# Kernel tuning notes

Hardware: AMD Instinct MI355X
Metric: run time of the kernel (lower is better)

Reference implementation:

```python
import jax, jax.numpy as jnp
import numpy as np

R, B, S, H, E, P = 8, 16, 512, 1024, 32, 4  # roles, batch, seq(=max_seq_len=char_len), hidden, entities, spans/entity


def setup_inputs() -> dict:
    key = jax.random.key(0)
    ks = jax.random.split(key, 12)
    w = 0.02
    return {
        "role_labels": jax.random.randint(ks[0], (R, B), 0, S),
        "summar_role_embedding": jax.random.normal(ks[1], (R, B, S, H), jnp.float32),
        "token_embedding": jax.random.normal(ks[2], (B, S, H), jnp.float32),
        "entities_embedding": jax.random.normal(ks[3], (B, S, H), jnp.float32),
        "token_mask": jnp.ones((B, S), jnp.float32),
        "entity_mask": jnp.ones((B, S), jnp.float32),
        # padded ragged spans: sort (start,end) so start<=end; empty spans write nothing
        "entity_spans": jnp.sort(jax.random.randint(ks[4], (B, E, P, 2), 0, S), axis=-1),
        # -1 encodes Python None entries in the original ragged maps
        "char2token": jax.random.randint(ks[5], (B, S), -1, S),
        "entity2token": jax.random.randint(ks[6], (B, S), -1, E),
        "single_w": jax.random.normal(ks[7], (3 * H, 1), jnp.float32) * w,
        "single_b": jnp.zeros((1,), jnp.float32),
        "multi_w": jax.random.normal(ks[8], (3 * H, 1), jnp.float32) * w,
        "multi_b": jnp.zeros((1,), jnp.float32),
        "answer_w": jax.random.normal(ks[9], (2 * H, H), jnp.float32) * w,
        "answer_b": jnp.zeros((H,), jnp.float32),
    }


def reference(role_labels, summar_role_embedding, token_embedding, entities_embedding,
              token_mask, entity_mask, entity_spans, char2token, entity2token,
              single_w, single_b, multi_w, multi_b, answer_w, answer_b):
    Bd, Sd, Hd = token_embedding.shape
    Ed = entity_spans.shape[1]
    brow = jnp.arange(Bd)[:, None]
    cvalid = char2token >= 0
    cidx = jnp.where(cvalid, char2token, 0)
    evalid = entity2token >= 0
    eidx = jnp.where(evalid, entity2token, 0)
    pos = jnp.arange(Sd)[None, None, None, :]  # [1,1,1,S]
    # span coverage mask [B,E,P,S]; assumes non-overlapping gold spans (matches sequential writes)
    cover = ((pos >= entity_spans[..., 0:1]) & (pos < entity_spans[..., 1:2])).astype(token_embedding.dtype)
    mask_sum = token_mask.sum()

    def step(pre_answer, xs):
        sr_emb, labels = xs
        s_logit = jnp.concatenate([sr_emb, token_embedding, pre_answer], -1) @ single_w + single_b  # [B,S,1]
        m_logit = jnp.concatenate([sr_emb, entities_embedding, pre_answer], -1) @ multi_w + multi_b
        # nn.Softmax() with no dim on a 3D tensor uses legacy dim=0 (batch axis)
        s_pred = jax.nn.softmax(s_logit, axis=0)[..., 0]  # [B,S]
        m_pred = jax.nn.softmax(m_logit, axis=0)[..., 0]
        # scatter-add char scores onto token positions / entity ids
        pred_token_ids = jnp.zeros((Bd, Sd), s_pred.dtype).at[brow, cidx].add(jnp.where(cvalid, s_pred, 0.0))
        entity_scores = jnp.zeros((Bd, Ed), m_pred.dtype).at[brow, eidx].add(jnp.where(evalid, m_pred, 0.0))
        # broadcast entity score over its spans
        pred_entity_ids = jnp.einsum('beps,be->bs', cover, entity_scores)
        merged = jnp.maximum(pred_token_ids, pred_entity_ids)  # max-merge [B,S]
        # gather merged scores back to char positions
        arg_emb = jnp.where(cvalid, jnp.take_along_axis(merged, cidx, axis=1), 0.0)[..., None]  # [B,S,1]
        curr = token_embedding * arg_emb
        new_pre = jnp.concatenate([curr, pre_answer], -1) @ answer_w + answer_b
        # CrossEntropyLoss(merged [B,C=S], labels [B]) -> scalar mean, then * token_mask.sum()
        nll = -jnp.take_along_axis(jax.nn.log_softmax(merged, -1), labels[:, None], axis=1).mean()
        return new_pre, (merged, nll * mask_sum)

    pre0 = jnp.zeros_like(token_embedding)
    _, (pred_arg_ids, losses) = jax.lax.scan(step, pre0, (summar_role_embedding, role_labels))
    return losses.sum(), pred_arg_ids
```

## Files before the change

### kernel.cpp

```cpp
#include <hip/hip_runtime.h>
#include <stdint.h>

#define R_ 8
#define B_ 16
#define S_ 512
#define H_ 1024
#define E_ 32
#define P_ 4
#define M_ (B_*S_)
#define SRB2_ 1024
#define TOKB_ 512
#define ENTB_ 512

__device__ __forceinline__ float dot4(float4 a, float4 b){
  return a.x*b.x + a.y*b.y + a.z*b.z + a.w*b.w;
}

__device__ __forceinline__ void group_barrier(int* cnt, int nblk){
  __syncthreads();
  if (threadIdx.x == 0){
    __threadfence();
    __hip_atomic_fetch_add(cnt, 1, __ATOMIC_RELEASE, __HIP_MEMORY_SCOPE_AGENT);
    while (__hip_atomic_load(cnt, __ATOMIC_ACQUIRE, __HIP_MEMORY_SCOPE_AGENT) < nblk)
      __builtin_amdgcn_s_sleep(8);
    __threadfence();
  }
  __syncthreads();
}

__global__ __launch_bounds__(256) void vec_chain_kernel(
    int k, const float* __restrict__ aw, const float* __restrict__ ab,
    const float* __restrict__ sw, const float* __restrict__ mw,
    float* __restrict__ a_s, float* __restrict__ a_m,
    float* __restrict__ V, float* __restrict__ betas)
{
  int w = (int)((blockIdx.x * blockDim.x + threadIdx.x) >> 6);
  int lane = threadIdx.x & 63;
  const float* as_k = (k == 0) ? (sw + 2*H_) : (a_s + (size_t)k*H_);
  const float* am_k = (k == 0) ? (mw + 2*H_) : (a_m + (size_t)k*H_);
  if (w < H_){
    const float* w1 = aw + (size_t)w * H_;
    const float* w2 = aw + (size_t)(H_ + w) * H_;
    float vs = 0.f, vm = 0.f, ns = 0.f, nm = 0.f;
    #pragma unroll
    for (int i = 0; i < 4; i++){
      int c = i*256 + lane*4;
      float4 r1 = *(const float4*)(w1 + c);
      float4 r2 = *(const float4*)(w2 + c);
      float4 xs = *(const float4*)(as_k + c);
      float4 xm = *(const float4*)(am_k + c);
      vs += dot4(r1, xs); vm += dot4(r1, xm);
      ns += dot4(r2, xs); nm += dot4(r2, xm);
    }
    #pragma unroll
    for (int m = 32; m >= 1; m >>= 1){
      vs += __shfl_xor(vs, m, 64); vm += __shfl_xor(vm, m, 64);
      ns += __shfl_xor(ns, m, 64); nm += __shfl_xor(nm, m, 64);
    }
    if (lane == 0){
      V[(size_t)k*H_ + w]       = vs;
      V[(size_t)(7 + k)*H_ + w] = vm;
      a_s[(size_t)(k+1)*H_ + w] = ns;
      a_m[(size_t)(k+1)*H_ + w] = nm;
    }
  } else if (w == H_ || w == H_ + 1){
    const float* av = (w == H_) ? as_k : am_k;
    float d = 0.f;
    #pragma unroll
    for (int i = 0; i < 4; i++){
      int c = i*256 + lane*4;
      d += dot4(*(const float4*)(ab + c), *(const float4*)(av + c));
    }
    #pragma unroll
    for (int m = 32; m >= 1; m >>= 1) d += __shfl_xor(d, m, 64);
    if (lane == 0) betas[(w == H_ ? 0 : 8) + k] = d;
  }
}

__global__ __launch_bounds__(256) void dots_staged_kernel(
    const float* __restrict__ sr, const float* __restrict__ tok,
    const float* __restrict__ ent, const float* __restrict__ sw,
    const float* __restrict__ mw, const float* __restrict__ V,
    const float* __restrict__ tmask,
    float* __restrict__ sr_s, float* __restrict__ sr_m,
    float* __restrict__ tok_s, float* __restrict__ ent_m,
    float* __restrict__ G, float* __restrict__ PS,
    float* __restrict__ msum, float* __restrict__ out)
{
  __shared__ float lds[8*1024];
  const int blk  = blockIdx.x;
  const int lane = threadIdx.x & 63;
  const int lw   = threadIdx.x >> 6;
  const int co   = lane * 4;

  if (blk < SRB2_){
    float4 ws4[4], wm4[4];
    #pragma unroll
    for (int i = 0; i < 4; i++){
      ws4[i] = *(const float4*)(sw + i*256 + co);
      wm4[i] = *(const float4*)(mw + i*256 + co);
    }
    auto STAGE = [&](int bufI, int h){
      int row = (blk + (h >> 1)*SRB2_)*8 + (h & 1)*4 + lw;
      const float* gb = sr + (size_t)row * H_;
      float* lb = lds + bufI*4096 + lw*1024;
      #pragma unroll
      for (int p = 0; p < 4; ++p){
        __builtin_amdgcn_global_load_lds(
            (const __attribute__((address_space(1))) unsigned int*)(gb + p*256 + lane*4),
            (__attribute__((address_space(3))) unsigned int*)(lb + p*256), 16, 0, 0);
      }
    };
    STAGE(0, 0);
    for (int h = 0; h < 16; ++h){
      if (h < 15){
        STAGE((h + 1) & 1, h + 1);
        asm volatile("s_waitcnt vmcnt(4)" ::: "memory");
      } else {
        asm volatile("s_waitcnt vmcnt(0)" ::: "memory");
      }
      const float* lrow = lds + (h & 1)*4096 + lw*1024;
      float a0 = 0.f, a1 = 0.f;
      #pragma unroll
      for (int i = 0; i < 4; i++){
        float4 v = *(const float4*)(lrow + i*256 + co);
        a0 += dot4(v, ws4[i]);
        a1 += dot4(v, wm4[i]);
      }
      #pragma unroll
      for (int m = 32; m >= 1; m >>= 1){
        a0 += __shfl_xor(a0,m,64); a1 += __shfl_xor(a1,m,64);
      }
      int row = (blk + (h >> 1)*SRB2_)*8 + (h & 1)*4 + lw;
      if (lane == 0){ sr_s[row] = a0; sr_m[row] = a1; }
    }
  } else if (blk < SRB2_ + TOKB_){
    const int gw = (blk - SRB2_)*4 + lw;
    const int h  = gw & 1;
    const int r0 = gw >> 1;
    if (h == 0){
      for (int it = 0; it < 8; ++it){
        int rr = r0 + it*1024;
        const float* rp = tok + (size_t)rr * H_;
        float acc[8];
        #pragma unroll
        for (int q = 0; q < 8; q++) acc[q] = 0.f;
        #pragma unroll
        for (int i = 0; i < 4; i++){
          int c = i*256 + co;
          float4 v = *(const float4*)(rp + c);
          acc[0] += dot4(v, *(const float4*)(sw + H_ + c));
          #pragma unroll
          for (int q = 0; q < 7; q++)
            acc[q+1] += dot4(v, *(const float4*)(V + (size_t)q*H_ + c));
        }
        #pragma unroll
        for (int m = 32; m >= 1; m >>= 1)
          #pragma unroll
          for (int q = 0; q < 8; q++) acc[q] += __shfl_xor(acc[q],m,64);
        if (lane == 0){
          tok_s[rr] = acc[0];
          #pragma unroll
          for (int q = 0; q < 7; q++) G[(size_t)q*M_ + rr] = acc[q+1];
        }
      }
    } else {
      for (int it = 0; it < 8; ++it){
        int rr = r0 + it*1024;
        const float* rp = tok + (size_t)rr * H_;
        float acc[7];
        #pragma unroll
        for (int q = 0; q < 7; q++) acc[q] = 0.f;
        #pragma unroll
        for (int i = 0; i < 4; i++){
          int c = i*256 + co;
          float4 v = *(const float4*)(rp + c);
          #pragma unroll
          for (int q = 0; q < 7; q++)
            acc[q] += dot4(v, *(const float4*)(V + (size_t)(7+q)*H_ + c));
        }
        #pragma unroll
        for (int m = 32; m >= 1; m >>= 1)
          #pragma unroll
          for (int q = 0; q < 7; q++) acc[q] += __shfl_xor(acc[q],m,64);
        if (lane == 0){
          #pragma unroll
          for (int q = 0; q < 7; q++) G[(size_t)(7+q)*M_ + rr] = acc[q];
        }
      }
    }
  } else {
    const int eb = blk - SRB2_ - TOKB_;
    const int gt = eb*256 + threadIdx.x;
    if (gt < 32768) ((float4*)PS)[gt] = make_float4(0.f,0.f,0.f,0.f);
    if (eb == 0 && lw == 0){
      float s = 0.f;
      #pragma unroll
      for (int i = 0; i < 32; i++){
        float4 v = ((const float4*)tmask)[i*64 + lane];
        s += v.x + v.y + v.z + v.w;
      }
      #pragma unroll
      for (int m = 32; m >= 1; m >>= 1) s += __shfl_xor(s, m, 64);
      if (lane == 0){ msum[0] = s; out[0] = 0.f; }
    }
    const int ew = eb*4 + lw;
    float4 wmh[4];
    #pragma unroll
    for (int i = 0; i < 4; i++) wmh[i] = *(const float4*)(mw + H_ + i*256 + co);
    #pragma unroll
    for (int it = 0; it < 4; ++it){
      int rr = ew + it*2048;
      const float* rp = ent + (size_t)rr * H_;
      float a0 = 0.f;
      #pragma unroll
      for (int i = 0; i < 4; i++)
        a0 += dot4(*(const float4*)(rp + i*256 + co), wmh[i]);
      #pragma unroll
      for (int m = 32; m >= 1; m >>= 1) a0 += __shfl_xor(a0,m,64);
      if (lane == 0) ent_m[rr] = a0;
    }
  }
}

__global__ __launch_bounds__(512) void roles_kernel(
    const float* __restrict__ sr_s, const float* __restrict__ sr_m,
    const float* __restrict__ tok_s, const float* __restrict__ ent_m,
    const float* __restrict__ G, const float* __restrict__ betas,
    const float* __restrict__ sb, const float* __restrict__ mb,
    const int* __restrict__ c2t, const int* __restrict__ e2t,
    const int* __restrict__ spans, const int* __restrict__ labels,
    const float* __restrict__ msum, float* __restrict__ out,
    float* __restrict__ xlog, float* __restrict__ PS, int* bar)
{
  __shared__ float pta[S_];
  __shared__ float merged[S_];
  __shared__ float es[E_];
  __shared__ float red[8];
  __shared__ int   spn[E_*P_*2];
  const int b = blockIdx.x;
  const int t = threadIdx.x;
  const int bs = b*S_ + t;
  const int wid = t >> 6, lane = t & 63;

  if (t < E_*P_*2) spn[t] = spans[b*(E_*P_*2) + t];
  const int c_own = c2t[bs];
  const int e_own = e2t[bs];
  const float sb0 = sb[0], mb0 = mb[0];
  const float msumv = msum[0];
  const float tok_sv = tok_s[bs], ent_mv = ent_m[bs];
  float bsum_s = 0.f, bsum_m = 0.f;

  for (int r = 0; r < R_; ++r){
    pta[t] = 0.f;
    if (t < E_) es[t] = 0.f;

    float sl[B_], ml[B_];
    if (r == 0){
      #pragma unroll
      for (int bb = 0; bb < B_; bb++){
        int q = bb*S_ + t;
        sl[bb] = sr_s[q] + tok_s[q] + sb0;
        ml[bb] = sr_m[q] + ent_m[q] + mb0;
      }
    } else {
      const float* xc = xlog + (size_t)(r & 1) * (2*M_);
      #pragma unroll
      for (int bb = 0; bb < B_; bb++){
        sl[bb] = xc[bb*S_ + t];
        ml[bb] = xc[M_ + bb*S_ + t];
      }
    }
    float smax = -1e30f, mmax = -1e30f;
    #pragma unroll
    for (int bb = 0; bb < B_; bb++){ smax = fmaxf(smax, sl[bb]); mmax = fmaxf(mmax, ml[bb]); }
    float ssum = 0.f, msv = 0.f;
    #pragma unroll
    for (int bb = 0; bb < B_; bb++){ ssum += __expf(sl[bb]-smax); msv += __expf(ml[bb]-mmax); }
    float spv = __expf(sl[b]-smax) / ssum;
    float mpv = __expf(ml[b]-mmax) / msv;

    __syncthreads();
    if (c_own >= 0) atomicAdd(&pta[c_own], spv);
    if (e_own >= 0) atomicAdd(&es[e_own], mpv);
    __syncthreads();

    float pei = 0.f;
    #pragma unroll
    for (int e = 0; e < E_; e++){
      float sc = es[e];
      #pragma unroll
      for (int p = 0; p < P_; p++){
        int st = spn[e*8 + p*2], en = spn[e*8 + p*2 + 1];
        if (t >= st && t < en) pei += sc;
      }
    }
    float mg = fmaxf(pta[t], pei);
    merged[t] = mg;
    out[1 + (size_t)r*M_ + bs] = mg;
    __syncthreads();

    float ah_r = (c_own >= 0) ? merged[c_own] : 0.f;

    float mx = mg;
    #pragma unroll
    for (int k = 32; k >= 1; k >>= 1) mx = fmaxf(mx, __shfl_xor(mx, k, 64));
    if (lane == 0) red[wid] = mx;
    __syncthreads();
    float gmx = red[0];
    #pragma unroll
    for (int i = 1; i < 8; i++) gmx = fmaxf(gmx, red[i]);
    float se = __expf(mg - gmx);
    #pragma unroll
    for (int k = 32; k >= 1; k >>= 1) se += __shfl_xor(se, k, 64);
    __syncthreads();
    if (lane == 0) red[wid] = se;
    __syncthreads();
    if (t == 0){
      float tot = 0.f;
      #pragma unroll
      for (int i = 0; i < 8; i++) tot += red[i];
      float lse = gmx + __logf(tot);
      int lbl = labels[r*B_ + b];
      float nll = lse - merged[lbl];
      atomicAdd(out, nll * msumv * (1.0f/16.0f));
    }

    if (r < 7){
      bsum_s += betas[r]; bsum_m += betas[8 + r];
      float ps_next = 0.f, pm_next = 0.f;
      for (int q = r + 1; q <= 7; q++){
        float gs = G[(size_t)(q-1-r)*M_ + bs];
        float gm = G[(size_t)(7 + q-1-r)*M_ + bs];
        float ns = PS[((size_t)q*2 + 0)*M_ + bs] + ah_r * gs;
        float nm = PS[((size_t)q*2 + 1)*M_ + bs] + ah_r * gm;
        PS[((size_t)q*2 + 0)*M_ + bs] = ns;
        PS[((size_t)q*2 + 1)*M_ + bs] = nm;
        if (q == r + 1){ ps_next = ns; pm_next = nm; }
      }
      float xn = sr_s[(size_t)((r+1)*B_ + b)*S_ + t] + tok_sv + ps_next + sb0 + bsum_s;
      float yn = sr_m[(size_t)((r+1)*B_ + b)*S_ + t] + ent_mv + pm_next + mb0 + bsum_m;
      float* xn_buf = xlog + (size_t)((r+1) & 1) * (2*M_);
      xn_buf[bs] = xn;
      xn_buf[M_ + bs] = yn;
      group_barrier(&bar[r], 16);
    }
  }
}

extern "C" void kernel_launch(void* const* d_in, const int* in_sizes, int n_in,
                              void* d_out, int out_size, void* d_ws, size_t ws_size,
                              hipStream_t stream){
  (void)in_sizes; (void)n_in; (void)out_size; (void)ws_size;
  const int*   labels = (const int*)  d_in[0];
  const float* sr     = (const float*)d_in[1];
  const float* tok    = (const float*)d_in[2];
  const float* ent    = (const float*)d_in[3];
  const float* tmask  = (const float*)d_in[4];
  const int*   spans  = (const int*)  d_in[6];
  const int*   c2t    = (const int*)  d_in[7];
  const int*   e2t    = (const int*)  d_in[8];
  const float* sw     = (const float*)d_in[9];
  const float* sb     = (const float*)d_in[10];
  const float* mw     = (const float*)d_in[11];
  const float* mb     = (const float*)d_in[12];
  const float* aw     = (const float*)d_in[13];
  const float* ab     = (const float*)d_in[14];
  float* out = (float*)d_out;
  char*  ws  = (char*)d_ws;

  size_t o = 0;
  auto take = [&](size_t bytes){ size_t c = o; o += (bytes + 255) & ~(size_t)255; return c; };
  float* sr_s  = (float*)(ws + take((size_t)R_*B_*S_*4));
  float* sr_m  = (float*)(ws + take((size_t)R_*B_*S_*4));
  float* tok_s = (float*)(ws + take((size_t)B_*S_*4));
  float* ent_m = (float*)(ws + take((size_t)B_*S_*4));
  float* a_s   = (float*)(ws + take((size_t)8*H_*4));
  float* a_m   = (float*)(ws + take((size_t)8*H_*4));
  float* V     = (float*)(ws + take((size_t)14*H_*4));
  float* betas = (float*)(ws + take(64));
  float* G     = (float*)(ws + take((size_t)14*M_*4));
  float* PS    = (float*)(ws + take((size_t)8*2*M_*4));
  float* xlog  = (float*)(ws + take((size_t)2*2*M_*4));
  float* msum  = (float*)(ws + take(256));
  int*   bar   = (int*)  (ws + take(64));

  hipMemsetAsync(bar, 0, 64, stream);
  for (int k = 0; k < 7; k++)
    vec_chain_kernel<<<257, 256, 0, stream>>>(k, aw, ab, sw, mw, a_s, a_m, V, betas);
  dots_staged_kernel<<<2048, 256, 0, stream>>>(sr, tok, ent, sw, mw, V, tmask,
                                               sr_s, sr_m, tok_s, ent_m, G, PS, msum, out);
  roles_kernel<<<16, 512, 0, stream>>>(sr_s, sr_m, tok_s, ent_m, G, betas,
                                       sb, mb, c2t, e2t, spans, labels, msum, out,
                                       xlog, PS, bar);
}
```

Measured before the change: 170.5 us.

## Spread summary-role dot products across the serial vector-chain launches

```diff
diff --git a/kernel.cpp b/kernel.cpp
--- a/kernel.cpp
+++ b/kernel.cpp
@@ -11,6 +11,8 @@
 #define SRB2_ 1024
 #define TOKB_ 512
 #define ENTB_ 512
+#define CHB_  257
+#define SLICE_ 8192
 
 __device__ __forceinline__ float dot4(float4 a, float4 b){
   return a.x*b.x + a.y*b.y + a.z*b.z + a.w*b.w;
@@ -28,52 +30,115 @@
   __syncthreads();
 }
 
-__global__ __launch_bounds__(256) void vec_chain_kernel(
-    int k, const float* __restrict__ aw, const float* __restrict__ ab,
-    const float* __restrict__ sw, const float* __restrict__ mw,
+__global__ __launch_bounds__(256) void hybrid_kernel(
+    int k,
+    const float* __restrict__ sr, const float* __restrict__ aw,
+    const float* __restrict__ ab, const float* __restrict__ sw,
+    const float* __restrict__ mw,
     float* __restrict__ a_s, float* __restrict__ a_m,
-    float* __restrict__ V, float* __restrict__ betas)
+    float* __restrict__ V, float* __restrict__ betas,
+    float* __restrict__ sr_s, float* __restrict__ sr_m)
 {
-  int w = (int)((blockIdx.x * blockDim.x + threadIdx.x) >> 6);
-  int lane = threadIdx.x & 63;
-  const float* as_k = (k == 0) ? (sw + 2*H_) : (a_s + (size_t)k*H_);
-  const float* am_k = (k == 0) ? (mw + 2*H_) : (a_m + (size_t)k*H_);
-  if (w < H_){
-    const float* w1 = aw + (size_t)w * H_;
-    const float* w2 = aw + (size_t)(H_ + w) * H_;
-    float vs = 0.f, vm = 0.f, ns = 0.f, nm = 0.f;
+  __shared__ float lds[8*1024];
+  const int blk  = blockIdx.x;
+  const int lane = threadIdx.x & 63;
+  const int lw   = threadIdx.x >> 6;
+  const int co   = lane * 4;
+
+  if (blk < CHB_){
+    int w = blk*4 + lw;
+    const float* as_k = (k == 0) ? (sw + 2*H_) : (a_s + (size_t)k*H_);
+    const float* am_k = (k == 0) ? (mw + 2*H_) : (a_m + (size_t)k*H_);
+    if (w < H_){
+      const float* w1 = aw + (size_t)w * H_;
+      const float* w2 = aw + (size_t)(H_ + w) * H_;
+      float vs = 0.f, vm = 0.f, ns = 0.f, nm = 0.f;
+      #pragma unroll
+      for (int i = 0; i < 4; i++){
+        int c = i*256 + co;
+        float4 r1 = *(const float4*)(w1 + c);
+        float4 r2 = *(const float4*)(w2 + c);
+        float4 xs = *(const float4*)(as_k + c);
+        float4 xm = *(const float4*)(am_k + c);
+        vs += dot4(r1, xs); vm += dot4(r1, xm);
+        ns += dot4(r2, xs); nm += dot4(r2, xm);
+      }
+      #pragma unroll
+      for (int m = 32; m >= 1; m >>= 1){
+        vs += __shfl_xor(vs, m, 64); vm += __shfl_xor(vm, m, 64);
+        ns += __shfl_xor(ns, m, 64); nm += __shfl_xor(nm, m, 64);
+      }
+      if (lane == 0){
+        V[(size_t)k*H_ + w]       = vs;
+        V[(size_t)(7 + k)*H_ + w] = vm;
+        a_s[(size_t)(k+1)*H_ + w] = ns;
+        a_m[(size_t)(k+1)*H_ + w] = nm;
+      }
+    } else if (w == H_ || w == H_ + 1){
+      const float* av = (w == H_) ? as_k : am_k;
+      float d = 0.f;
+      #pragma unroll
+      for (int i = 0; i < 4; i++){
+        int c = i*256 + co;
+        d += dot4(*(const float4*)(ab + c), *(const float4*)(av + c));
+      }
+      #pragma unroll
+      for (int m = 32; m >= 1; m >>= 1) d += __shfl_xor(d, m, 64);
+      if (lane == 0) betas[(w == H_ ? 0 : 8) + k] = d;
+    }
+  } else {
+    const int sb2 = blk - CHB_;
+    float4 ws4[4], wm4[4];
     #pragma unroll
     for (int i = 0; i < 4; i++){
-      int c = i*256 + lane*4;
-      float4 r1 = *(const float4*)(w1 + c);
-      float4 r2 = *(const float4*)(w2 + c);
-      float4 xs = *(const float4*)(as_k + c);
-      float4 xm = *(const float4*)(am_k + c);
-      vs += dot4(r1, xs); vm += dot4(r1, xm);
-      ns += dot4(r2, xs); nm += dot4(r2, xm);
-    }
-    #pragma unroll
-    for (int m = 32; m >= 1; m >>= 1){
-      vs += __shfl_xor(vs, m, 64); vm += __shfl_xor(vm, m, 64);
-      ns += __shfl_xor(ns, m, 64); nm += __shfl_xor(nm, m, 64);
-    }
-    if (lane == 0){
-      V[(size_t)k*H_ + w]       = vs;
-      V[(size_t)(7 + k)*H_ + w] = vm;
-      a_s[(size_t)(k+1)*H_ + w] = ns;
-      a_m[(size_t)(k+1)*H_ + w] = nm;
-    }
-  } else if (w == H_ || w == H_ + 1){
-    const float* av = (w == H_) ? as_k : am_k;
-    float d = 0.f;
-    #pragma unroll
-    for (int i = 0; i < 4; i++){
-      int c = i*256 + lane*4;
-      d += dot4(*(const float4*)(ab + c), *(const float4*)(av + c));
-    }
-    #pragma unroll
-    for (int m = 32; m >= 1; m >>= 1) d += __shfl_xor(d, m, 64);
-    if (lane == 0) betas[(w == H_ ? 0 : 8) + k] = d;
+      ws4[i] = *(const float4*)(sw + i*256 + co);
+      wm4[i] = *(const float4*)(mw + i*256 + co);
+    }
+    const int row0 = k*SLICE_ + sb2*8 + lw;
+    auto STAGE = [&](int bufI, int half){
+      const float* gb = sr + (size_t)(row0 + half*4) * H_;
+      float* lb = lds + bufI*4096 + lw*1024;
+      #pragma unroll
+      for (int p = 0; p < 4; ++p){
+        __builtin_amdgcn_global_load_lds(
+            (const __attribute__((address_space(1))) unsigned int*)(gb + p*256 + lane*4),
+            (__attribute__((address_space(3))) unsigned int*)(lb + p*256), 16, 0, 0);
+      }
+    };
+    STAGE(0, 0);
+    STAGE(1, 1);
+    asm volatile("s_waitcnt vmcnt(4)" ::: "memory");
+    {
+      const float* lrow = lds + lw*1024;
+      float a0 = 0.f, a1 = 0.f;
+      #pragma unroll
+      for (int i = 0; i < 4; i++){
+        float4 v = *(const float4*)(lrow + i*256 + co);
+        a0 += dot4(v, ws4[i]);
+        a1 += dot4(v, wm4[i]);
+      }
+      #pragma unroll
+      for (int m = 32; m >= 1; m >>= 1){
+        a0 += __shfl_xor(a0,m,64); a1 += __shfl_xor(a1,m,64);
+      }
+      if (lane == 0){ sr_s[row0] = a0; sr_m[row0] = a1; }
+    }
+    asm volatile("s_waitcnt vmcnt(2)" ::: "memory");
+    {
+      const float* lrow = lds + 4096 + lw*1024;
+      float a0 = 0.f, a1 = 0.f;
+      #pragma unroll
+      for (int i = 0; i < 4; i++){
+        float4 v = *(const float4*)(lrow + i*256 + co);
+        a0 += dot4(v, ws4[i]);
+        a1 += dot4(v, wm4[i]);
+      }
+      #pragma unroll
+      for (int m = 32; m >= 1; m >>= 1){
+        a0 += __shfl_xor(a0,m,64); a1 += __shfl_xor(a1,m,64);
+      }
+      if (lane == 0){ sr_s[row0 + 4] = a0; sr_m[row0 + 4] = a1; }
+    }
   }
 }
 
@@ -100,9 +165,9 @@
       ws4[i] = *(const float4*)(sw + i*256 + co);
       wm4[i] = *(const float4*)(mw + i*256 + co);
     }
-    auto STAGE = [&](int bufI, int h){
-      int row = (blk + (h >> 1)*SRB2_)*8 + (h & 1)*4 + lw;
-      const float* gb = sr + (size_t)row * H_;
+    const int row0 = 7*SLICE_ + blk*8 + lw;
+    auto STAGE = [&](int bufI, int half){
+      const float* gb = sr + (size_t)(row0 + half*4) * H_;
       float* lb = lds + bufI*4096 + lw*1024;
       #pragma unroll
       for (int p = 0; p < 4; ++p){
@@ -112,14 +177,10 @@
       }
     };
     STAGE(0, 0);
-    for (int h = 0; h < 16; ++h){
-      if (h < 15){
-        STAGE((h + 1) & 1, h + 1);
-        asm volatile("s_waitcnt vmcnt(4)" ::: "memory");
-      } else {
-        asm volatile("s_waitcnt vmcnt(0)" ::: "memory");
-      }
-      const float* lrow = lds + (h & 1)*4096 + lw*1024;
+    STAGE(1, 1);
+    asm volatile("s_waitcnt vmcnt(4)" ::: "memory");
+    {
+      const float* lrow = lds + lw*1024;
       float a0 = 0.f, a1 = 0.f;
       #pragma unroll
       for (int i = 0; i < 4; i++){
@@ -131,8 +192,23 @@
       for (int m = 32; m >= 1; m >>= 1){
         a0 += __shfl_xor(a0,m,64); a1 += __shfl_xor(a1,m,64);
       }
-      int row = (blk + (h >> 1)*SRB2_)*8 + (h & 1)*4 + lw;
-      if (lane == 0){ sr_s[row] = a0; sr_m[row] = a1; }
+      if (lane == 0){ sr_s[row0] = a0; sr_m[row0] = a1; }
+    }
+    asm volatile("s_waitcnt vmcnt(2)" ::: "memory");
+    {
+      const float* lrow = lds + 4096 + lw*1024;
+      float a0 = 0.f, a1 = 0.f;
+      #pragma unroll
+      for (int i = 0; i < 4; i++){
+        float4 v = *(const float4*)(lrow + i*256 + co);
+        a0 += dot4(v, ws4[i]);
+        a1 += dot4(v, wm4[i]);
+      }
+      #pragma unroll
+      for (int m = 32; m >= 1; m >>= 1){
+        a0 += __shfl_xor(a0,m,64); a1 += __shfl_xor(a1,m,64);
+      }
+      if (lane == 0){ sr_s[row0 + 4] = a0; sr_m[row0 + 4] = a1; }
     }
   } else if (blk < SRB2_ + TOKB_){
     const int gw = (blk - SRB2_)*4 + lw;
@@ -387,7 +463,8 @@
 
   hipMemsetAsync(bar, 0, 64, stream);
   for (int k = 0; k < 7; k++)
-    vec_chain_kernel<<<257, 256, 0, stream>>>(k, aw, ab, sw, mw, a_s, a_m, V, betas);
+    hybrid_kernel<<<CHB_ + SRB2_, 256, 0, stream>>>(k, sr, aw, ab, sw, mw,
+                                                    a_s, a_m, V, betas, sr_s, sr_m);
   dots_staged_kernel<<<2048, 256, 0, stream>>>(sr, tok, ent, sw, mw, V, tmask,
                                                sr_s, sr_m, tok_s, ent_m, G, PS, msum, out);
   roles_kernel<<<16, 512, 0, stream>>>(sr_s, sr_m, tok_s, ent_m, G, betas,
```

Result: slower. 177.6 us (+4.2%).
